# Optimization experiments

Measured on AMD Instinct MI355X. Metric: run time of the kernel, lower is better.

Reference implementation:

```python
import jax, jax.numpy as jnp
import numpy as np

N_NODES = 100000
N_EDGES = 1600000
N_GRAPHS = 64
DIMS = [128, 128, 128, 128]
IN_CH = 4


def setup_inputs() -> dict:
    key = jax.random.key(0)
    ks = jax.random.split(key, 24)
    d = {}
    d['x'] = jax.random.normal(ks[0], (N_NODES, IN_CH), dtype=jnp.float32)
    d['metadata'] = jax.random.normal(ks[1], (N_GRAPHS, 1), dtype=jnp.float32)
    d['edge_index'] = jax.random.randint(ks[2], (2, N_EDGES), 0, N_NODES, dtype=jnp.int32)
    d['batch'] = jnp.sort(jax.random.randint(ks[3], (N_NODES,), 0, N_GRAPHS, dtype=jnp.int32))
    dims_in = [IN_CH] + DIMS[:-1]
    ki = 4
    for i, (din, dout) in enumerate(zip(dims_in, DIMS), start=1):
        s = 1.0 / np.sqrt(din)
        d[f'w_rel{i}'] = jax.random.normal(ks[ki], (din, dout), dtype=jnp.float32) * s; ki += 1
        d[f'b_rel{i}'] = jnp.zeros((dout,), dtype=jnp.float32)
        d[f'w_root{i}'] = jax.random.normal(ks[ki], (din, dout), dtype=jnp.float32) * s; ki += 1
    d['convm_w'] = jax.random.normal(ks[ki], (4,), dtype=jnp.float32); ki += 1
    d['convm_b'] = jnp.zeros((4,), dtype=jnp.float32)
    fin = DIMS[3] * 2 + 4
    d['fc_w'] = jax.random.normal(ks[ki], (fin, DIMS[3]), dtype=jnp.float32) / np.sqrt(fin); ki += 1
    d['fc_b'] = jnp.zeros((DIMS[3],), dtype=jnp.float32)
    d['fc2_w'] = jax.random.normal(ks[ki], (DIMS[3], 1), dtype=jnp.float32) / np.sqrt(DIMS[3]); ki += 1
    d['fc2_b'] = jnp.zeros((1,), dtype=jnp.float32)
    return d


def _graph_conv(x, src, dst, w_rel, b_rel, w_root):
    # PyG GraphConv (aggr='add'): out_i = lin_rel(sum_{j->i} x_j) + lin_root(x_i)
    agg = jax.ops.segment_sum(x[src], dst, num_segments=N_NODES)
    return agg @ w_rel + b_rel + x @ w_root


def reference(x, metadata, edge_index, batch,
              w_rel1, b_rel1, w_root1,
              w_rel2, b_rel2, w_root2,
              w_rel3, b_rel3, w_root3,
              w_rel4, b_rel4, w_root4,
              convm_w, convm_b, fc_w, fc_b, fc2_w, fc2_b):
    src, dst = edge_index[0], edge_index[1]
    h = jax.nn.relu(_graph_conv(x, src, dst, w_rel1, b_rel1, w_root1))
    h = jax.nn.relu(_graph_conv(h, src, dst, w_rel2, b_rel2, w_root2))
    h = jax.nn.relu(_graph_conv(h, src, dst, w_rel3, b_rel3, w_root3))
    h = jax.nn.relu(_graph_conv(h, src, dst, w_rel4, b_rel4, w_root4))
    # global pools per graph
    counts = jax.ops.segment_sum(jnp.ones((N_NODES,), h.dtype), batch, num_segments=N_GRAPHS)
    x_sum = jax.ops.segment_sum(h, batch, num_segments=N_GRAPHS)
    x_mean = x_sum / jnp.maximum(counts, 1.0)[:, None]
    x_max = jax.ops.segment_max(h, batch, num_segments=N_GRAPHS)
    x_max = jnp.where(counts[:, None] > 0, x_max, 0.0)
    # metadata branch: Conv1d(1,4,k=1) on [B,1,1] -> [B,4]
    m = jax.nn.relu(metadata * convm_w[None, :] + convm_b[None, :])  # [B,4]
    x_c = jnp.concatenate([x_max, x_mean, m], axis=1)  # [B, 2*d+4]
    out = jax.nn.relu(x_c @ fc_w + fc_b) @ fc2_w + fc2_b
    return out[:, 0]
```

## Files before the change

### kernel.cpp

```cpp
#include <hip/hip_runtime.h>

#define N_NODES 100000
#define N_EDGES 1600000
#define N_GRAPHS 64

__device__ __forceinline__ unsigned int f2bf(float f) {
  unsigned int u = __float_as_uint(f);
  return (u + 0x7FFFu + ((u >> 16) & 1u)) >> 16;
}
#define BLO(u) __uint_as_float((u) << 16)
#define BHI(u) __uint_as_float((u) & 0xFFFF0000u)


__global__ __launch_bounds__(256) void k_zero_int(int* __restrict__ p, int n) {
  int i = blockIdx.x * 256 + threadIdx.x;
  if (i < n) p[i] = 0;
}

__global__ __launch_bounds__(256) void k_hist(const int* __restrict__ ei, int* __restrict__ deg) {
  int e = blockIdx.x * 256 + threadIdx.x;
  if (e < N_EDGES) atomicAdd(&deg[ei[N_EDGES + e]], 1);
}

__global__ __launch_bounds__(256) void k_scan1(const int* __restrict__ deg, int* __restrict__ part,
                                               int* __restrict__ bsum) {
  __shared__ int tmp[256];
  int i = blockIdx.x * 256 + threadIdx.x;
  int v = (i < N_NODES) ? deg[i] : 0;
  tmp[threadIdx.x] = v;
  __syncthreads();
  for (int o = 1; o < 256; o <<= 1) {
    int t = (threadIdx.x >= o) ? tmp[threadIdx.x - o] : 0;
    __syncthreads();
    tmp[threadIdx.x] += t;
    __syncthreads();
  }
  if (i < N_NODES) part[i] = tmp[threadIdx.x] - v;
  if (threadIdx.x == 255) bsum[blockIdx.x] = tmp[255];
}

__global__ __launch_bounds__(512) void k_scan2(const int* __restrict__ bsum, int* __restrict__ boff, int nb) {
  __shared__ int tmp[512];
  int v = ((int)threadIdx.x < nb) ? bsum[threadIdx.x] : 0;
  tmp[threadIdx.x] = v;
  __syncthreads();
  for (int o = 1; o < 512; o <<= 1) {
    int t = (threadIdx.x >= o) ? tmp[threadIdx.x - o] : 0;
    __syncthreads();
    tmp[threadIdx.x] += t;
    __syncthreads();
  }
  if ((int)threadIdx.x < nb) boff[threadIdx.x] = tmp[threadIdx.x] - v;
}

__global__ __launch_bounds__(256) void k_scan3(const int* __restrict__ part, const int* __restrict__ boff,
                                               int* __restrict__ rowptr, int* __restrict__ cursor) {
  int i = blockIdx.x * 256 + threadIdx.x;
  if (i < N_NODES) {
    int r = part[i] + boff[i >> 8];
    rowptr[i] = r;
    cursor[i] = r;
  } else if (i == N_NODES) {
    rowptr[N_NODES] = N_EDGES;
  }
}

#define FW_NPW 12500
#define FW_EPS 12500
__global__ __launch_bounds__(256) void k_fill_win(const int* __restrict__ ei, int* __restrict__ cursor,
                                                  int* __restrict__ csr) {
  int bid = blockIdx.x;
  int w = bid & 7;
  int s = bid >> 3;
  int lo = w * FW_NPW, hi = lo + FW_NPW;
  int e0 = s * FW_EPS, e1 = e0 + FW_EPS;
  for (int e = e0 + threadIdx.x; e < e1; e += 256) {
    int d = ei[N_EDGES + e];
    if (d >= lo && d < hi) {
      int p = atomicAdd(&cursor[d], 1);
      csr[p] = ei[e];
    }
  }
}


__global__ __launch_bounds__(256) void k_l1_agg(const float* __restrict__ x, const int* __restrict__ rowptr,
                                                const int* __restrict__ csr, float* __restrict__ agg4) {
  int t = blockIdx.x * 256 + threadIdx.x;
  if (t >= N_NODES * 4) return;
  int node = t >> 2, c = t & 3;
  int s = rowptr[node], e = rowptr[node + 1];
  float a = 0.f;
  for (int p = s; p < e; ++p) a += x[(size_t)csr[p] * 4 + c];
  agg4[t] = a;
}

__global__ __launch_bounds__(256) void k_l1_comb(const float* __restrict__ x, const float* __restrict__ agg4,
                                                 const float* __restrict__ w_rel, const float* __restrict__ b_rel,
                                                 const float* __restrict__ w_root, float* __restrict__ out,
                                                 unsigned short* __restrict__ hb) {
  int t = blockIdx.x * 256 + threadIdx.x;
  int node = t >> 7, c = t & 127;
  if (node >= N_NODES) return;
  float acc = b_rel[c];
#pragma unroll
  for (int k = 0; k < 4; ++k) acc += agg4[node * 4 + k] * w_rel[k * 128 + c];
#pragma unroll
  for (int k = 0; k < 4; ++k) acc += x[node * 4 + k] * w_root[k * 128 + c];
  float r = fmaxf(acc, 0.f);
  out[(size_t)node * 128 + c] = r;
  hb[(size_t)node * 128 + c] = (unsigned short)f2bf(r);
}

#define AGG_ACC(U)                                                    \
  a0.x += BLO((U).x); a0.y += BHI((U).x);                             \
  a0.z += BLO((U).y); a0.w += BHI((U).y);                             \
  a1.x += BLO((U).z); a1.y += BHI((U).z);                             \
  a1.z += BLO((U).w); a1.w += BHI((U).w);

__global__ __launch_bounds__(256) void k_agg_bf(const unsigned short* __restrict__ hb,
                                                const int* __restrict__ rowptr, const int* __restrict__ csr,
                                                float* __restrict__ aggout) {
  int node = (blockIdx.x * 256 + threadIdx.x) >> 4;
  int l = threadIdx.x & 15;
  if (node >= N_NODES) return;
  int s = rowptr[node], e = rowptr[node + 1];
  float4 a0 = make_float4(0.f, 0.f, 0.f, 0.f);
  float4 a1 = make_float4(0.f, 0.f, 0.f, 0.f);
  int p = s;
  for (; p + 4 <= e; p += 4) {
    int s0 = csr[p], s1 = csr[p + 1], s2 = csr[p + 2], s3 = csr[p + 3];
    uint4 u0 = *(const uint4*)&hb[(size_t)s0 * 128 + l * 8];
    uint4 u1 = *(const uint4*)&hb[(size_t)s1 * 128 + l * 8];
    uint4 u2 = *(const uint4*)&hb[(size_t)s2 * 128 + l * 8];
    uint4 u3 = *(const uint4*)&hb[(size_t)s3 * 128 + l * 8];
    AGG_ACC(u0)
    AGG_ACC(u1)
    AGG_ACC(u2)
    AGG_ACC(u3)
  }
  for (; p < e; ++p) {
    int s0 = csr[p];
    uint4 u = *(const uint4*)&hb[(size_t)s0 * 128 + l * 8];
    AGG_ACC(u)
  }
  *(float4*)&aggout[(size_t)node * 128 + l * 8] = a0;
  *(float4*)&aggout[(size_t)node * 128 + l * 8 + 4] = a1;
}

#define GEMM_STEP(AV, M)                                                                   \
  acc[M][0].x += (AV)*b0.x; acc[M][0].y += (AV)*b0.y;                                      \
  acc[M][0].z += (AV)*b0.z; acc[M][0].w += (AV)*b0.w;                                      \
  acc[M][1].x += (AV)*b1.x; acc[M][1].y += (AV)*b1.y;                                      \
  acc[M][1].z += (AV)*b1.z; acc[M][1].w += (AV)*b1.w;

__global__ __launch_bounds__(256) void k_gemm4(const float* __restrict__ agg, const float* __restrict__ h,
                                               const float* __restrict__ w_rel, const float* __restrict__ w_root,
                                               const float* __restrict__ bias, float* __restrict__ out,
                                               unsigned short* __restrict__ hb) {
  __shared__ float AsT[32][128];
  __shared__ float Bs[32][128];
  const int n0 = blockIdx.x * 128;
  const int tid = threadIdx.x;
  const int tr = tid >> 4;
  const int tc = tid & 15;
  float4 acc[8][2];
#pragma unroll
  for (int m = 0; m < 8; ++m) {
    acc[m][0] = make_float4(0.f, 0.f, 0.f, 0.f);
    acc[m][1] = make_float4(0.f, 0.f, 0.f, 0.f);
  }

  for (int chunk = 0; chunk < 2; ++chunk) {
    const float* src = (chunk == 0) ? agg : h;
    const float* wgt = (chunk == 0) ? w_rel : w_root;
    for (int k0 = 0; k0 < 128; k0 += 32) {
#pragma unroll
      for (int t = 0; t < 4; ++t) {
        int idx = tid + t * 256;
        int r = idx & 127, q = idx >> 7;
        int gr = n0 + r;
        if (gr >= N_NODES) gr = N_NODES - 1;
        float4 v = *(const float4*)&src[(size_t)gr * 128 + k0 + q * 4];
        AsT[q * 4 + 0][r] = v.x;
        AsT[q * 4 + 1][r] = v.y;
        AsT[q * 4 + 2][r] = v.z;
        AsT[q * 4 + 3][r] = v.w;
      }
#pragma unroll
      for (int t = 0; t < 4; ++t) {
        int idx = tid + t * 256;
        int k = idx >> 5, cq = idx & 31;
        *(float4*)&Bs[k][cq * 4] = *(const float4*)&wgt[(size_t)(k0 + k) * 128 + cq * 4];
      }
      __syncthreads();
#pragma unroll 4
      for (int k = 0; k < 32; ++k) {
        float4 a0 = *(float4*)&AsT[k][tr * 8];
        float4 a1 = *(float4*)&AsT[k][tr * 8 + 4];
        float4 b0 = *(float4*)&Bs[k][tc * 4];
        float4 b1 = *(float4*)&Bs[k][tc * 4 + 64];
        GEMM_STEP(a0.x, 0)
        GEMM_STEP(a0.y, 1)
        GEMM_STEP(a0.z, 2)
        GEMM_STEP(a0.w, 3)
        GEMM_STEP(a1.x, 4)
        GEMM_STEP(a1.y, 5)
        GEMM_STEP(a1.z, 6)
        GEMM_STEP(a1.w, 7)
      }
      __syncthreads();
    }
  }

  float4 bi0 = *(const float4*)&bias[tc * 4];
  float4 bi1 = *(const float4*)&bias[tc * 4 + 64];
#pragma unroll
  for (int m = 0; m < 8; ++m) {
    int row = n0 + tr * 8 + m;
    if (row < N_NODES) {
      float4 o0, o1;
      o0.x = fmaxf(acc[m][0].x + bi0.x, 0.f);
      o0.y = fmaxf(acc[m][0].y + bi0.y, 0.f);
      o0.z = fmaxf(acc[m][0].z + bi0.z, 0.f);
      o0.w = fmaxf(acc[m][0].w + bi0.w, 0.f);
      o1.x = fmaxf(acc[m][1].x + bi1.x, 0.f);
      o1.y = fmaxf(acc[m][1].y + bi1.y, 0.f);
      o1.z = fmaxf(acc[m][1].z + bi1.z, 0.f);
      o1.w = fmaxf(acc[m][1].w + bi1.w, 0.f);
      *(float4*)&out[(size_t)row * 128 + tc * 4] = o0;
      *(float4*)&out[(size_t)row * 128 + tc * 4 + 64] = o1;
      uint2 pA, pB;
      pA.x = f2bf(o0.x) | (f2bf(o0.y) << 16);
      pA.y = f2bf(o0.z) | (f2bf(o0.w) << 16);
      pB.x = f2bf(o1.x) | (f2bf(o1.y) << 16);
      pB.y = f2bf(o1.z) | (f2bf(o1.w) << 16);
      *(uint2*)&hb[(size_t)row * 128 + tc * 4] = pA;
      *(uint2*)&hb[(size_t)row * 128 + tc * 4 + 64] = pB;
    }
  }
}


__device__ __forceinline__ int lower_bound_batch(const int* __restrict__ batch, int key) {
  int lo = 0, hi = N_NODES;
  while (lo < hi) {
    int mid = (lo + hi) >> 1;
    if (batch[mid] < key) lo = mid + 1;
    else hi = mid;
  }
  return lo;
}

__global__ __launch_bounds__(256) void k_pool1(const float* __restrict__ h, const int* __restrict__ batch,
                                               float* __restrict__ psum, float* __restrict__ pmax) {
  int b = blockIdx.x;
  int g = b >> 2, q = b & 3;
  int start = lower_bound_batch(batch, g);
  int end = lower_bound_batch(batch, g + 1);
  int c = threadIdx.x & 127;
  int half = threadIdx.x >> 7;
  float sum = 0.f, mx = -3.0e38f;
  for (int n = start + q * 2 + half; n < end; n += 8) {
    float v = h[(size_t)n * 128 + c];
    sum += v;
    mx = fmaxf(mx, v);
  }
  __shared__ float ss[128], sm[128];
  if (half == 0) { ss[c] = sum; sm[c] = mx; }
  __syncthreads();
  if (half == 1) { ss[c] += sum; sm[c] = fmaxf(sm[c], mx); }
  __syncthreads();
  if (half == 0) {
    psum[(size_t)b * 128 + c] = ss[c];
    pmax[(size_t)b * 128 + c] = sm[c];
  }
}

__global__ __launch_bounds__(128) void k_pool2(const float* __restrict__ psum, const float* __restrict__ pmax,
                                               const int* __restrict__ batch, float* __restrict__ pooled) {
  int g = blockIdx.x;
  int c = threadIdx.x;
  int start = lower_bound_batch(batch, g), end = lower_bound_batch(batch, g + 1);
  int count = end - start;
  float s = 0.f, m = -3.0e38f;
#pragma unroll
  for (int q = 0; q < 4; ++q) {
    s += psum[(size_t)(g * 4 + q) * 128 + c];
    m = fmaxf(m, pmax[(size_t)(g * 4 + q) * 128 + c]);
  }
  pooled[(size_t)g * 256 + c] = (count > 0) ? m : 0.f;
  pooled[(size_t)g * 256 + 128 + c] = s / fmaxf((float)count, 1.f);
}


__global__ __launch_bounds__(128) void k_fc(const float* __restrict__ pooled, const float* __restrict__ metadata,
                                            const float* __restrict__ convm_w, const float* __restrict__ convm_b,
                                            const float* __restrict__ fc_w, const float* __restrict__ fc_b,
                                            const float* __restrict__ fc2_w, const float* __restrict__ fc2_b,
                                            float* __restrict__ out) {
  int g = blockIdx.x;
  int tid = threadIdx.x;
  __shared__ float xc[260];
  xc[tid] = pooled[(size_t)g * 256 + tid];
  xc[128 + tid] = pooled[(size_t)g * 256 + 128 + tid];
  if (tid < 4) xc[256 + tid] = fmaxf(metadata[g] * convm_w[tid] + convm_b[tid], 0.f);
  __syncthreads();
  float acc = fc_b[tid];
  for (int k = 0; k < 260; ++k) acc += xc[k] * fc_w[(size_t)k * 128 + tid];
  float partial = fmaxf(acc, 0.f) * fc2_w[tid];
#pragma unroll
  for (int off = 32; off > 0; off >>= 1) partial += __shfl_down(partial, off);
  __shared__ float wred[2];
  if ((tid & 63) == 0) wred[tid >> 6] = partial;
  __syncthreads();
  if (tid == 0) out[g] = wred[0] + wred[1] + fc2_b[0];
}


extern "C" void kernel_launch(void* const* d_in, const int* in_sizes, int n_in,
                              void* d_out, int out_size, void* d_ws, size_t ws_size,
                              hipStream_t stream) {
  const float* x = (const float*)d_in[0];
  const float* metadata = (const float*)d_in[1];
  const int* ei = (const int*)d_in[2];
  const int* batch = (const int*)d_in[3];
  const float* w_rel[4] = {(const float*)d_in[4], (const float*)d_in[7], (const float*)d_in[10], (const float*)d_in[13]};
  const float* b_rel[4] = {(const float*)d_in[5], (const float*)d_in[8], (const float*)d_in[11], (const float*)d_in[14]};
  const float* w_root[4] = {(const float*)d_in[6], (const float*)d_in[9], (const float*)d_in[12], (const float*)d_in[15]};
  const float* convm_w = (const float*)d_in[16];
  const float* convm_b = (const float*)d_in[17];
  const float* fc_w = (const float*)d_in[18];
  const float* fc_b = (const float*)d_in[19];
  const float* fc2_w = (const float*)d_in[20];
  const float* fc2_b = (const float*)d_in[21];
  float* out = (float*)d_out;

  char* ws = (char*)d_ws;
  size_t off = 0;
  auto alloc = [&](size_t bytes) {
    off = (off + 255) & ~(size_t)255;
    void* p = ws + off;
    off += bytes;
    return p;
  };
  int* deg = (int*)alloc((size_t)N_NODES * 4);
  int* rowptr = (int*)alloc((size_t)(N_NODES + 1) * 4);
  int* cursor = (int*)alloc((size_t)N_NODES * 4);
  int* bsum = (int*)alloc(512 * 4);
  int* boff = (int*)alloc(512 * 4);
  int* csr = (int*)alloc((size_t)N_EDGES * 4);
  float* agg4 = (float*)alloc((size_t)N_NODES * 4 * 4);
  float* bufA = (float*)alloc((size_t)N_NODES * 128 * 4);
  float* bufB = (float*)alloc((size_t)N_NODES * 128 * 4);
  unsigned short* hb = (unsigned short*)alloc((size_t)N_NODES * 128 * 2);
  float* psum = (float*)alloc((size_t)256 * 128 * 4);
  float* pmax = (float*)alloc((size_t)256 * 128 * 4);
  float* pooled = (float*)alloc((size_t)64 * 256 * 4);

  const int nblk_nodes = (N_NODES + 255) / 256;
  const int nblk_edges = (N_EDGES + 255) / 256;

  k_zero_int<<<nblk_nodes, 256, 0, stream>>>(deg, N_NODES);
  k_hist<<<nblk_edges, 256, 0, stream>>>(ei, deg);
  k_scan1<<<nblk_nodes, 256, 0, stream>>>(deg, rowptr, bsum);
  k_scan2<<<1, 512, 0, stream>>>(bsum, boff, nblk_nodes);
  k_scan3<<<(N_NODES + 1 + 255) / 256, 256, 0, stream>>>(rowptr, boff, rowptr, cursor);
  k_fill_win<<<8 * 128, 256, 0, stream>>>(ei, cursor, csr);

  k_l1_agg<<<(N_NODES * 4 + 255) / 256, 256, 0, stream>>>(x, rowptr, csr, agg4);
  k_l1_comb<<<(N_NODES * 128 + 255) / 256, 256, 0, stream>>>(x, agg4, w_rel[0], b_rel[0], w_root[0], bufA, hb);

  for (int l = 1; l < 4; ++l) {
    k_agg_bf<<<(N_NODES * 16 + 255) / 256, 256, 0, stream>>>(hb, rowptr, csr, bufB);
    k_gemm4<<<(N_NODES + 127) / 128, 256, 0, stream>>>(bufB, bufA, w_rel[l], w_root[l], b_rel[l], bufA, hb);
  }

  k_pool1<<<256, 256, 0, stream>>>(bufA, batch, psum, pmax);
  k_pool2<<<64, 128, 0, stream>>>(psum, pmax, batch, pooled);
  k_fc<<<64, 128, 0, stream>>>(pooled, metadata, convm_w, convm_b, fc_w, fc_b, fc2_w, fc2_b, out);
}
```

Baseline: 872.2 us.

## Replace FP32 SIMT GEMM with split-bf16 MFMA GEMM and pre-transposed weights

Swaps the shared-memory FP32 FMA GEMM for a matrix-core kernel using 16x16x32 bf16 MFMA. A three-term hi/lo bf16 split keeps near-FP32 accuracy, and a new prep kernel converts and transposes the weights into bf16 hi/lo form. The last layer also skips writing the bf16 copy of the hidden state. The costs are three MFMAs per product, per-lane conversion of A, direct global loads of weights with no LDS, and uncoalesced scalar output stores.

```diff
diff --git a/kernel.cpp b/kernel.cpp
--- a/kernel.cpp
+++ b/kernel.cpp
@@ -4,12 +4,32 @@
 #define N_EDGES 1600000
 #define N_GRAPHS 64
 
+typedef __attribute__((ext_vector_type(8))) short bf16x8;
+typedef __attribute__((ext_vector_type(4))) float f32x4;
+
 __device__ __forceinline__ unsigned int f2bf(float f) {
   unsigned int u = __float_as_uint(f);
   return (u + 0x7FFFu + ((u >> 16) & 1u)) >> 16;
 }
 #define BLO(u) __uint_as_float((u) << 16)
 #define BHI(u) __uint_as_float((u) & 0xFFFF0000u)
+
+__device__ __forceinline__ void split8(const float* __restrict__ p, bf16x8& hi, bf16x8& lo) {
+  float4 v0 = *(const float4*)p;
+  float4 v1 = *(const float4*)(p + 4);
+  unsigned h0 = f2bf(v0.x), h1 = f2bf(v0.y), h2 = f2bf(v0.z), h3 = f2bf(v0.w);
+  unsigned h4 = f2bf(v1.x), h5 = f2bf(v1.y), h6 = f2bf(v1.z), h7 = f2bf(v1.w);
+  hi[0] = (short)h0; hi[1] = (short)h1; hi[2] = (short)h2; hi[3] = (short)h3;
+  hi[4] = (short)h4; hi[5] = (short)h5; hi[6] = (short)h6; hi[7] = (short)h7;
+  lo[0] = (short)f2bf(v0.x - __uint_as_float(h0 << 16));
+  lo[1] = (short)f2bf(v0.y - __uint_as_float(h1 << 16));
+  lo[2] = (short)f2bf(v0.z - __uint_as_float(h2 << 16));
+  lo[3] = (short)f2bf(v0.w - __uint_as_float(h3 << 16));
+  lo[4] = (short)f2bf(v1.x - __uint_as_float(h4 << 16));
+  lo[5] = (short)f2bf(v1.y - __uint_as_float(h5 << 16));
+  lo[6] = (short)f2bf(v1.z - __uint_as_float(h6 << 16));
+  lo[7] = (short)f2bf(v1.w - __uint_as_float(h7 << 16));
+}
 
 
 __global__ __launch_bounds__(256) void k_zero_int(int* __restrict__ p, int n) {
@@ -81,6 +101,17 @@
       csr[p] = ei[e];
     }
   }
+}
+
+__global__ __launch_bounds__(256) void k_prep_w(const float* __restrict__ w, unsigned short* __restrict__ wt) {
+  int t = blockIdx.x * 256 + threadIdx.x;
+  int k = t >> 7, c = t & 127;
+  float v = w[k * 128 + c];
+  unsigned int hi = f2bf(v);
+  float vhi = __uint_as_float(hi << 16);
+  unsigned int lo = f2bf(v - vhi);
+  wt[c * 256 + k] = (unsigned short)hi;
+  wt[c * 256 + k + 128] = (unsigned short)lo;
 }
 
 
@@ -148,95 +179,72 @@
   *(float4*)&aggout[(size_t)node * 128 + l * 8 + 4] = a1;
 }
 
-#define GEMM_STEP(AV, M)                                                                   \
-  acc[M][0].x += (AV)*b0.x; acc[M][0].y += (AV)*b0.y;                                      \
-  acc[M][0].z += (AV)*b0.z; acc[M][0].w += (AV)*b0.w;                                      \
-  acc[M][1].x += (AV)*b1.x; acc[M][1].y += (AV)*b1.y;                                      \
-  acc[M][1].z += (AV)*b1.z; acc[M][1].w += (AV)*b1.w;
-
-__global__ __launch_bounds__(256) void k_gemm4(const float* __restrict__ agg, const float* __restrict__ h,
-                                               const float* __restrict__ w_rel, const float* __restrict__ w_root,
-                                               const float* __restrict__ bias, float* __restrict__ out,
-                                               unsigned short* __restrict__ hb) {
-  __shared__ float AsT[32][128];
-  __shared__ float Bs[32][128];
-  const int n0 = blockIdx.x * 128;
+__global__ __launch_bounds__(256) void k_gemm_mfma2(
+    const float* __restrict__ agg, const float* __restrict__ h,
+    const unsigned short* __restrict__ wrelT, const unsigned short* __restrict__ wrootT,
+    const float* __restrict__ bias, const int last,
+    float* __restrict__ hout, unsigned short* __restrict__ hbout) {
   const int tid = threadIdx.x;
-  const int tr = tid >> 4;
-  const int tc = tid & 15;
-  float4 acc[8][2];
-#pragma unroll
-  for (int m = 0; m < 8; ++m) {
-    acc[m][0] = make_float4(0.f, 0.f, 0.f, 0.f);
-    acc[m][1] = make_float4(0.f, 0.f, 0.f, 0.f);
-  }
-
-  for (int chunk = 0; chunk < 2; ++chunk) {
-    const float* src = (chunk == 0) ? agg : h;
-    const float* wgt = (chunk == 0) ? w_rel : w_root;
-    for (int k0 = 0; k0 < 128; k0 += 32) {
-#pragma unroll
-      for (int t = 0; t < 4; ++t) {
-        int idx = tid + t * 256;
-        int r = idx & 127, q = idx >> 7;
-        int gr = n0 + r;
-        if (gr >= N_NODES) gr = N_NODES - 1;
-        float4 v = *(const float4*)&src[(size_t)gr * 128 + k0 + q * 4];
-        AsT[q * 4 + 0][r] = v.x;
-        AsT[q * 4 + 1][r] = v.y;
-        AsT[q * 4 + 2][r] = v.z;
-        AsT[q * 4 + 3][r] = v.w;
+  const int wave = tid >> 6;
+  const int lane = tid & 63;
+  const int l15 = lane & 15;
+  const int lg = lane >> 4;
+  const int rb = blockIdx.x * 64 + wave * 16;
+  int ar = rb + l15;
+  if (ar >= N_NODES) ar = N_NODES - 1;
+
+  f32x4 acc[8];
+#pragma unroll
+  for (int i = 0; i < 8; ++i) acc[i] = (f32x4){0.f, 0.f, 0.f, 0.f};
+
+#pragma unroll
+  for (int src = 0; src < 2; ++src) {
+    const float* A = src ? h : agg;
+    const unsigned short* W = src ? wrootT : wrelT;
+    const float* arow = A + (size_t)ar * 128 + lg * 8;
+    bf16x8 ah0, al0, ah1, al1, ah2, al2, ah3, al3;
+    split8(arow, ah0, al0);
+    split8(arow + 32, ah1, al1);
+    split8(arow + 64, ah2, al2);
+    split8(arow + 96, ah3, al3);
+#pragma unroll
+    for (int c0 = 0; c0 < 8; ++c0) {
+      const unsigned short* wc = W + (size_t)(c0 * 16 + l15) * 256 + lg * 8;
+      bf16x8 bh0 = *(const bf16x8*)(wc);
+      bf16x8 bh1 = *(const bf16x8*)(wc + 32);
+      bf16x8 bh2 = *(const bf16x8*)(wc + 64);
+      bf16x8 bh3 = *(const bf16x8*)(wc + 96);
+      bf16x8 bl0 = *(const bf16x8*)(wc + 128);
+      bf16x8 bl1 = *(const bf16x8*)(wc + 160);
+      bf16x8 bl2 = *(const bf16x8*)(wc + 192);
+      bf16x8 bl3 = *(const bf16x8*)(wc + 224);
+      acc[c0] = __builtin_amdgcn_mfma_f32_16x16x32_bf16(ah0, bh0, acc[c0], 0, 0, 0);
+      acc[c0] = __builtin_amdgcn_mfma_f32_16x16x32_bf16(ah1, bh1, acc[c0], 0, 0, 0);
+      acc[c0] = __builtin_amdgcn_mfma_f32_16x16x32_bf16(ah2, bh2, acc[c0], 0, 0, 0);
+      acc[c0] = __builtin_amdgcn_mfma_f32_16x16x32_bf16(ah3, bh3, acc[c0], 0, 0, 0);
+      acc[c0] = __builtin_amdgcn_mfma_f32_16x16x32_bf16(ah0, bl0, acc[c0], 0, 0, 0);
+      acc[c0] = __builtin_amdgcn_mfma_f32_16x16x32_bf16(ah1, bl1, acc[c0], 0, 0, 0);
+      acc[c0] = __builtin_amdgcn_mfma_f32_16x16x32_bf16(ah2, bl2, acc[c0], 0, 0, 0);
+      acc[c0] = __builtin_amdgcn_mfma_f32_16x16x32_bf16(ah3, bl3, acc[c0], 0, 0, 0);
+      acc[c0] = __builtin_amdgcn_mfma_f32_16x16x32_bf16(al0, bh0, acc[c0], 0, 0, 0);
+      acc[c0] = __builtin_amdgcn_mfma_f32_16x16x32_bf16(al1, bh1, acc[c0], 0, 0, 0);
+      acc[c0] = __builtin_amdgcn_mfma_f32_16x16x32_bf16(al2, bh2, acc[c0], 0, 0, 0);
+      acc[c0] = __builtin_amdgcn_mfma_f32_16x16x32_bf16(al3, bh3, acc[c0], 0, 0, 0);
+    }
+  }
+
+#pragma unroll
+  for (int c0 = 0; c0 < 8; ++c0) {
+    const int c = c0 * 16 + l15;
+    const float bi = bias[c];
+#pragma unroll
+    for (int j = 0; j < 4; ++j) {
+      const int row = rb + lg * 4 + j;
+      if (row < N_NODES) {
+        float v = fmaxf(acc[c0][j] + bi, 0.f);
+        hout[(size_t)row * 128 + c] = v;
+        if (!last) hbout[(size_t)row * 128 + c] = (unsigned short)f2bf(v);
       }
-#pragma unroll
-      for (int t = 0; t < 4; ++t) {
-        int idx = tid + t * 256;
-        int k = idx >> 5, cq = idx & 31;
-        *(float4*)&Bs[k][cq * 4] = *(const float4*)&wgt[(size_t)(k0 + k) * 128 + cq * 4];
-      }
-      __syncthreads();
-#pragma unroll 4
-      for (int k = 0; k < 32; ++k) {
-        float4 a0 = *(float4*)&AsT[k][tr * 8];
-        float4 a1 = *(float4*)&AsT[k][tr * 8 + 4];
-        float4 b0 = *(float4*)&Bs[k][tc * 4];
-        float4 b1 = *(float4*)&Bs[k][tc * 4 + 64];
-        GEMM_STEP(a0.x, 0)
-        GEMM_STEP(a0.y, 1)
-        GEMM_STEP(a0.z, 2)
-        GEMM_STEP(a0.w, 3)
-        GEMM_STEP(a1.x, 4)
-        GEMM_STEP(a1.y, 5)
-        GEMM_STEP(a1.z, 6)
-        GEMM_STEP(a1.w, 7)
-      }
-      __syncthreads();
-    }
-  }
-
-  float4 bi0 = *(const float4*)&bias[tc * 4];
-  float4 bi1 = *(const float4*)&bias[tc * 4 + 64];
-#pragma unroll
-  for (int m = 0; m < 8; ++m) {
-    int row = n0 + tr * 8 + m;
-    if (row < N_NODES) {
-      float4 o0, o1;
-      o0.x = fmaxf(acc[m][0].x + bi0.x, 0.f);
-      o0.y = fmaxf(acc[m][0].y + bi0.y, 0.f);
-      o0.z = fmaxf(acc[m][0].z + bi0.z, 0.f);
-      o0.w = fmaxf(acc[m][0].w + bi0.w, 0.f);
-      o1.x = fmaxf(acc[m][1].x + bi1.x, 0.f);
-      o1.y = fmaxf(acc[m][1].y + bi1.y, 0.f);
-      o1.z = fmaxf(acc[m][1].z + bi1.z, 0.f);
-      o1.w = fmaxf(acc[m][1].w + bi1.w, 0.f);
-      *(float4*)&out[(size_t)row * 128 + tc * 4] = o0;
-      *(float4*)&out[(size_t)row * 128 + tc * 4 + 64] = o1;
-      uint2 pA, pB;
-      pA.x = f2bf(o0.x) | (f2bf(o0.y) << 16);
-      pA.y = f2bf(o0.z) | (f2bf(o0.w) << 16);
-      pB.x = f2bf(o1.x) | (f2bf(o1.y) << 16);
-      pB.y = f2bf(o1.z) | (f2bf(o1.w) << 16);
-      *(uint2*)&hb[(size_t)row * 128 + tc * 4] = pA;
-      *(uint2*)&hb[(size_t)row * 128 + tc * 4 + 64] = pB;
     }
   }
 }
@@ -354,12 +362,18 @@
   float* bufA = (float*)alloc((size_t)N_NODES * 128 * 4);
   float* bufB = (float*)alloc((size_t)N_NODES * 128 * 4);
   unsigned short* hb = (unsigned short*)alloc((size_t)N_NODES * 128 * 2);
+  unsigned short* wt = (unsigned short*)alloc((size_t)6 * 128 * 256 * 2);
   float* psum = (float*)alloc((size_t)256 * 128 * 4);
   float* pmax = (float*)alloc((size_t)256 * 128 * 4);
   float* pooled = (float*)alloc((size_t)64 * 256 * 4);
 
   const int nblk_nodes = (N_NODES + 255) / 256;
   const int nblk_edges = (N_EDGES + 255) / 256;
+
+  for (int l = 1; l < 4; ++l) {
+    k_prep_w<<<64, 256, 0, stream>>>(w_rel[l], wt + (size_t)(2 * (l - 1)) * 32768);
+    k_prep_w<<<64, 256, 0, stream>>>(w_root[l], wt + (size_t)(2 * (l - 1) + 1) * 32768);
+  }
 
   k_zero_int<<<nblk_nodes, 256, 0, stream>>>(deg, N_NODES);
   k_hist<<<nblk_edges, 256, 0, stream>>>(ei, deg);
@@ -373,7 +387,9 @@
 
   for (int l = 1; l < 4; ++l) {
     k_agg_bf<<<(N_NODES * 16 + 255) / 256, 256, 0, stream>>>(hb, rowptr, csr, bufB);
-    k_gemm4<<<(N_NODES + 127) / 128, 256, 0, stream>>>(bufB, bufA, w_rel[l], w_root[l], b_rel[l], bufA, hb);
+    k_gemm_mfma2<<<(N_NODES + 63) / 64, 256, 0, stream>>>(
+        bufB, bufA, wt + (size_t)(2 * (l - 1)) * 32768, wt + (size_t)(2 * (l - 1) + 1) * 32768,
+        b_rel[l], (l == 3) ? 1 : 0, bufA, hb);
   }
 
   k_pool1<<<256, 256, 0, stream>>>(bufA, batch, psum, pmax);
```

New measurement: 969.6 us. 1.11x slower.
